# Optimization experiments

Measured on AMD Instinct MI355X. Metric: run time of the kernel, lower is better.

The kernel has to match this reference:

```python
import jax, jax.numpy as jnp
import numpy as np

B, T, D = 4, 2048, 1024
H, Dh = 16, 64
Q_LAT, KV_LAT, O_LAT = 512, 256, 512
ROPE = 32
FFN_RANK, FFN_INTER = 384, 4096
EPS = 1e-6
THETA = 10000.0


def rms_norm(x, w, eps=EPS):
    xf = x.astype(jnp.float32)
    var = jnp.mean(xf * xf, axis=-1, keepdims=True)
    return (w * (xf * jax.lax.rsqrt(var + eps))).astype(x.dtype)


def rotate_half(x):
    x1, x2 = jnp.split(x, 2, axis=-1)
    return jnp.concatenate([-x2, x1], axis=-1)


def setup_inputs() -> dict:
    key = jax.random.key(0)
    ks = jax.random.split(key, 12)
    s = lambda fan_in: 1.0 / np.sqrt(fan_in)
    inp = {
        "hidden_states": jax.random.normal(ks[0], (B, T, D), jnp.float32),
        "ln1_w": jnp.ones((D,), jnp.float32),
        "a_ln_w": jnp.ones((Q_LAT + KV_LAT,), jnp.float32),
        "qkv_a_w": jax.random.normal(ks[1], (D, Q_LAT + KV_LAT), jnp.float32) * s(D),
        "q_b_w": jax.random.normal(ks[2], (Q_LAT, H * Dh), jnp.float32) * s(Q_LAT),
        "kv_b_w": jax.random.normal(ks[3], (KV_LAT, 2 * H * Dh), jnp.float32) * s(KV_LAT),
        "o_a_w": jax.random.normal(ks[4], (H * Dh, O_LAT), jnp.float32) * s(H * Dh),
        "o_b_w": jax.random.normal(ks[5], (O_LAT, D), jnp.float32) * s(O_LAT),
        "ln2_w": jnp.ones((D,), jnp.float32),
        "ffn_in_a": jax.random.normal(ks[6], (D, FFN_RANK), jnp.float32) * s(D),
        "ffn_in_b": jax.random.normal(ks[7], (FFN_RANK, FFN_INTER), jnp.float32) * s(FFN_RANK),
        "ffn_out_a": jax.random.normal(ks[8], (FFN_INTER, FFN_RANK), jnp.float32) * s(FFN_INTER),
        "ffn_out_b": jax.random.normal(ks[9], (FFN_RANK, D), jnp.float32) * s(FFN_RANK),
    }
    # RoPE tables over first ROPE dims of each head
    inv_freq = 1.0 / (THETA ** (np.arange(0, ROPE, 2, dtype=np.float32) / ROPE))
    t = np.arange(T, dtype=np.float32)
    freqs = np.outer(t, inv_freq)                      # [T, ROPE/2]
    emb = np.concatenate([freqs, freqs], axis=-1)      # [T, ROPE]
    inp["cos"] = jnp.asarray(np.cos(emb), jnp.float32)
    inp["sin"] = jnp.asarray(np.sin(emb), jnp.float32)
    return inp


def reference(hidden_states, cos, sin, ln1_w, a_ln_w, qkv_a_w, q_b_w, kv_b_w,
              o_a_w, o_b_w, ln2_w, ffn_in_a, ffn_in_b, ffn_out_a, ffn_out_b):
    x = hidden_states
    # --- MLA attention (pre-norm) ---
    h = rms_norm(x, ln1_w)
    lat = rms_norm(h @ qkv_a_w, a_ln_w)                # [B,T,Q_LAT+KV_LAT]
    q_lat, kv_lat = jnp.split(lat, [Q_LAT], axis=-1)
    q = (q_lat @ q_b_w).reshape(B, T, H, Dh).transpose(0, 2, 1, 3)   # [B,H,T,Dh]
    kv = (kv_lat @ kv_b_w).reshape(B, T, H, 2 * Dh).transpose(0, 2, 1, 3)
    k, v = jnp.split(kv, 2, axis=-1)
    # partial RoPE on first ROPE dims
    c = cos[None, None]; s_ = sin[None, None]          # [1,1,T,ROPE]
    q_r, q_p = q[..., :ROPE], q[..., ROPE:]
    k_r, k_p = k[..., :ROPE], k[..., ROPE:]
    q = jnp.concatenate([q_r * c + rotate_half(q_r) * s_, q_p], axis=-1)
    k = jnp.concatenate([k_r * c + rotate_half(k_r) * s_, k_p], axis=-1)
    scores = jnp.einsum("bhqd,bhkd->bhqk", q, k) * (Dh ** -0.5)
    attn = jax.nn.softmax(scores, axis=-1)
    ctx = jnp.einsum("bhqk,bhkd->bhqd", attn, v)
    ctx = ctx.transpose(0, 2, 1, 3).reshape(B, T, H * Dh)
    attn_out = (ctx @ o_a_w) @ o_b_w                   # output subspace
    x = x + attn_out
    # --- decomposed FFN (pre-norm) ---
    h2 = rms_norm(x, ln2_w)
    ff = jax.nn.gelu((h2 @ ffn_in_a) @ ffn_in_b)
    ff = (ff @ ffn_out_a) @ ffn_out_b
    return x + ff
```

## Files before the change

### kernel.cpp

```cpp
#include <hip/hip_runtime.h>
#include <hip/hip_bf16.h>
#include <stdint.h>

#define NTOK 8192

typedef unsigned short u16;
typedef __attribute__((ext_vector_type(4))) float f32x4;
typedef __attribute__((ext_vector_type(8))) short s16x8;
typedef __attribute__((ext_vector_type(8))) u16   u16x8;
typedef __attribute__((ext_vector_type(4))) u16   u16x4;

__device__ __forceinline__ float fast_exp2(float x) {
    return __builtin_amdgcn_exp2f(x);
}
__device__ __forceinline__ u16 f2bf(float f) {
    uint32_t u = __float_as_uint(f);
    u = (u + 0x7FFFu + ((u >> 16) & 1u)) >> 16;
    return (u16)u;
}
__device__ __forceinline__ u16 f2bf_fast(float f) {
    return (u16)((__float_as_uint(f) + 0x8000u) >> 16);
}
__device__ __forceinline__ float bf2f(u16 h) {
    return __uint_as_float(((uint32_t)h) << 16);
}
__device__ __forceinline__ void async_cp16(const void* g, void* l) {
    __builtin_amdgcn_global_load_lds(
        (const __attribute__((address_space(1))) void*)g,
        (__attribute__((address_space(3))) void*)l, 16, 0, 0);
}
__device__ __forceinline__ void wait_vm4()   { asm volatile("s_waitcnt vmcnt(4)" ::: "memory"); }
__device__ __forceinline__ void wait_vm0()   { asm volatile("s_waitcnt vmcnt(0)" ::: "memory"); }
__device__ __forceinline__ void wait_lgkm0() { asm volatile("s_waitcnt lgkmcnt(0)" ::: "memory"); }
__device__ __forceinline__ void raw_barrier(){ asm volatile("s_barrier" ::: "memory"); }

struct TDesc { const float* s; u16* d; int K; int N; int tile0; };
struct TPack { TDesc t[8]; };

__global__ __launch_bounds__(256) void k_transpose_all(TPack p)
{
    __shared__ float tile[32][33];
    int bid = blockIdx.x;
    int i = 0;
    #pragma unroll
    for (int j = 1; j < 8; j++) if (bid >= p.t[j].tile0) i = j;
    const float* src = p.t[i].s;
    u16* dst = p.t[i].d;
    int K = p.t[i].K, N = p.t[i].N;
    int local = bid - p.t[i].tile0;
    int nx = N >> 5;
    int n0 = (local % nx) * 32, k0 = (local / nx) * 32;
    int tx = threadIdx.x, ty = threadIdx.y;
    #pragma unroll
    for (int r = 0; r < 32; r += 8)
        tile[ty + r][tx] = src[(size_t)(k0 + ty + r) * N + n0 + tx];
    __syncthreads();
    #pragma unroll
    for (int r = 0; r < 32; r += 8)
        dst[(size_t)(n0 + ty + r) * K + k0 + tx] = f2bf(tile[tx][ty + r]);
}

__global__ __launch_bounds__(256) void k_cvt(
    const float* __restrict__ in, u16* __restrict__ out)
{
    int i = (blockIdx.x * 256 + threadIdx.x) * 4;
    f32x4 v = *(const f32x4*)&in[i];
    u16x4 o;
    #pragma unroll
    for (int j = 0; j < 4; j++) o[j] = f2bf(v[j]);
    *(u16x4*)&out[i] = o;
}

template<int W>
__global__ __launch_bounds__(256) void k_rmsnorm(
    const float* __restrict__ x, const float* __restrict__ w, u16* __restrict__ out)
{
    constexpr int E = W / 256;
    int row = blockIdx.x, tid = threadIdx.x;
    const float* xr = x + (size_t)row * W;
    float v[E]; float ss = 0.f;
    #pragma unroll
    for (int i = 0; i < E; i++) { v[i] = xr[tid + i * 256]; ss += v[i] * v[i]; }
    #pragma unroll
    for (int m = 1; m < 64; m <<= 1) ss += __shfl_xor(ss, m, 64);
    __shared__ float red[4];
    if ((tid & 63) == 0) red[tid >> 6] = ss;
    __syncthreads();
    ss = red[0] + red[1] + red[2] + red[3];
    float scale = rsqrtf(ss / (float)W + 1e-6f);
    u16* orow = out + (size_t)row * W;
    #pragma unroll
    for (int i = 0; i < E; i++)
        orow[tid + i * 256] = f2bf(w[tid + i * 256] * (v[i] * scale));
}

template<int EPI>
__global__ __launch_bounds__(256) void k_gemm(
    const u16* __restrict__ A, int lda,
    const u16* __restrict__ Bt, int ldb,
    int M, int N, int K,
    float* __restrict__ outF, u16* __restrict__ outB,
    const float* __restrict__ resid)
{
    __shared__ __align__(16) u16 As[2][4096];
    __shared__ __align__(16) u16 Bs[2][4096];
    int tid = threadIdx.x;
    int w = tid >> 6, lane = tid & 63;
    int m0 = blockIdx.y * 128, n0 = blockIdx.x * 128;
    int wm = w & 1, wn = w >> 1;
    int lr = lane & 15, lq = lane >> 4;

    f32x4 acc[4][4];
    #pragma unroll
    for (int i = 0; i < 4; i++)
        #pragma unroll
        for (int j = 0; j < 4; j++) acc[i][j] = (f32x4)(0.f);

    int ar = tid >> 2;
    int ac = (tid & 3) * 8;
    const u16* Ag = A  + (size_t)(m0 + ar) * lda + ac;
    const u16* Bg = Bt + (size_t)(n0 + ar) * ldb + ac;
    int lo = w * 512;

    auto stage = [&](int kt, int s) {
        const u16* a  = Ag + kt * 32;
        const u16* bp = Bg + kt * 32;
        async_cp16(a,                     &As[s][lo]);
        async_cp16(a + (size_t)64 * lda,  &As[s][lo + 2048]);
        async_cp16(bp,                    &Bs[s][lo]);
        async_cp16(bp + (size_t)64 * ldb, &Bs[s][lo + 2048]);
    };

    int nk = K >> 5;
    stage(0, 0);
    stage(1, 1);
    for (int k = 0; k < nk; k++) {
        if (k + 1 < nk) wait_vm4(); else wait_vm0();
        raw_barrier();
        int s = k & 1;
        s16x8 af[4], bfr[4];
        #pragma unroll
        for (int ms = 0; ms < 4; ms++)
            af[ms] = *reinterpret_cast<const s16x8*>(&As[s][(wm * 64 + ms * 16 + lr) * 32 + lq * 8]);
        #pragma unroll
        for (int ns = 0; ns < 4; ns++)
            bfr[ns] = *reinterpret_cast<const s16x8*>(&Bs[s][(wn * 64 + ns * 16 + lr) * 32 + lq * 8]);
        #pragma unroll
        for (int ms = 0; ms < 4; ms++)
            #pragma unroll
            for (int ns = 0; ns < 4; ns++)
                acc[ms][ns] = __builtin_amdgcn_mfma_f32_16x16x32_bf16(af[ms], bfr[ns], acc[ms][ns], 0, 0, 0);
        wait_lgkm0();
        raw_barrier();
        if (k + 2 < nk) stage(k + 2, s);
    }

    #pragma unroll
    for (int ms = 0; ms < 4; ms++) {
        #pragma unroll
        for (int ns = 0; ns < 4; ns++) {
            int col = n0 + wn * 64 + ns * 16 + lr;
            #pragma unroll
            for (int r = 0; r < 4; r++) {
                int row = m0 + wm * 64 + ms * 16 + lq * 4 + r;
                float v = acc[ms][ns][r];
                size_t idx = (size_t)row * N + col;
                if (EPI == 0) {
                    outF[idx] = v;
                } else if (EPI == 1) {
                    outB[idx] = f2bf(v);
                } else if (EPI == 2) {
                    float t = 0.7978845608028654f * (v + 0.044715f * v * v * v);
                    outB[idx] = f2bf(0.5f * v * (1.f + tanhf(t)));
                } else {
                    outF[idx] = v + resid[idx];
                }
            }
        }
    }
}

template<int EPI>
__global__ __launch_bounds__(256) void k_gemm64(
    const u16* __restrict__ A, int lda,
    const u16* __restrict__ Bt, int ldb,
    int M, int N, int K,
    float* __restrict__ outF, u16* __restrict__ outB)
{
    __shared__ __align__(16) u16 As[2][4096];
    __shared__ __align__(16) u16 Bs[2][4096];
    int tid = threadIdx.x;
    int w = tid >> 6, lane = tid & 63;
    int m0 = blockIdx.y * 64, n0 = blockIdx.x * 64;
    int wm = w & 1, wn = w >> 1;
    int lr = lane & 15, lq = lane >> 4;

    f32x4 acc[2][2];
    #pragma unroll
    for (int i = 0; i < 2; i++)
        #pragma unroll
        for (int j = 0; j < 2; j++) acc[i][j] = (f32x4)(0.f);

    int srow = tid >> 2;
    int sq   = tid & 3;
    const u16* Ag = A  + (size_t)(m0 + srow) * lda + sq * 8;
    const u16* Bg = Bt + (size_t)(n0 + srow) * ldb + sq * 8;
    int lo = srow * 32 + sq * 8;

    auto stage = [&](int kt, int s) {
        const u16* a  = Ag + kt * 64;
        const u16* bp = Bg + kt * 64;
        async_cp16(a,       &As[s][lo]);
        async_cp16(a + 32,  &As[s][2048 + lo]);
        async_cp16(bp,      &Bs[s][lo]);
        async_cp16(bp + 32, &Bs[s][2048 + lo]);
    };

    int nk = K >> 6;
    stage(0, 0);
    stage(1, 1);
    for (int k = 0; k < nk; k++) {
        if (k + 1 < nk) wait_vm4(); else wait_vm0();
        raw_barrier();
        int s = k & 1;
        s16x8 af[2][2], bfr[2][2];
        #pragma unroll
        for (int kc = 0; kc < 2; kc++) {
            #pragma unroll
            for (int ms = 0; ms < 2; ms++)
                af[ms][kc] = *reinterpret_cast<const s16x8*>(
                    &As[s][kc * 2048 + (wm * 32 + ms * 16 + lr) * 32 + lq * 8]);
            #pragma unroll
            for (int ns = 0; ns < 2; ns++)
                bfr[ns][kc] = *reinterpret_cast<const s16x8*>(
                    &Bs[s][kc * 2048 + (wn * 32 + ns * 16 + lr) * 32 + lq * 8]);
        }
        #pragma unroll
        for (int kc = 0; kc < 2; kc++)
            #pragma unroll
            for (int ms = 0; ms < 2; ms++)
                #pragma unroll
                for (int ns = 0; ns < 2; ns++)
                    acc[ms][ns] = __builtin_amdgcn_mfma_f32_16x16x32_bf16(
                        af[ms][kc], bfr[ns][kc], acc[ms][ns], 0, 0, 0);
        wait_lgkm0();
        raw_barrier();
        if (k + 2 < nk) stage(k + 2, s);
    }

    #pragma unroll
    for (int ms = 0; ms < 2; ms++) {
        #pragma unroll
        for (int ns = 0; ns < 2; ns++) {
            int col = n0 + wn * 32 + ns * 16 + lr;
            #pragma unroll
            for (int r = 0; r < 4; r++) {
                int row = m0 + wm * 32 + ms * 16 + lq * 4 + r;
                float v = acc[ms][ns][r];
                size_t idx = (size_t)row * N + col;
                if (EPI == 0) outF[idx] = v;
                else          outB[idx] = f2bf(v);
            }
        }
    }
}

__global__ __launch_bounds__(256) void k_rope(
    const u16* __restrict__ q, const u16* __restrict__ kv,
    const float* __restrict__ cosb, const float* __restrict__ sinb,
    u16* __restrict__ q_r, u16* __restrict__ k_r)
{
    const float QS = 0.125f * 1.4426950408889634f;
    int idx = blockIdx.x * 256 + threadIdx.x;
    int g = idx & 7;
    int h = (idx >> 3) & 15;
    int t = (idx >> 7) & 2047;
    int b = idx >> 18;
    size_t qsrc = ((size_t)((b * 2048 + t) * 16 + h)) * 64 + g * 8;
    size_t ksrc = ((size_t)((b * 2048 + t) * 16 + h)) * 128 + g * 8;
    u16x8 qa = *(const u16x8*)&q[qsrc];
    u16x8 ka = *(const u16x8*)&kv[ksrc];
    u16x8 qo, ko;
    if (g < 4) {
        int pd = ((g ^ 2) - g) * 8;
        u16x8 qp = *(const u16x8*)&q[qsrc + pd];
        u16x8 kp = *(const u16x8*)&kv[ksrc + pd];
        float sgn = (g < 2) ? -1.f : 1.f;
        const float* cp = &cosb[t * 32 + g * 8];
        const float* sp = &sinb[t * 32 + g * 8];
        #pragma unroll
        for (int j = 0; j < 8; j++) {
            float c = cp[j], s = sp[j];
            qo[j] = f2bf((bf2f(qa[j]) * c + sgn * bf2f(qp[j]) * s) * QS);
            ko[j] = f2bf(bf2f(ka[j]) * c + sgn * bf2f(kp[j]) * s);
        }
    } else {
        #pragma unroll
        for (int j = 0; j < 8; j++) {
            qo[j] = f2bf(bf2f(qa[j]) * QS);
            ko[j] = ka[j];
        }
    }
    size_t dst = ((size_t)(b * 16 + h) * 2048 + t) * 64 + g * 8;
    *(u16x8*)&q_r[dst] = qo;
    *(u16x8*)&k_r[dst] = ko;
}

__global__ __launch_bounds__(256) void k_vtrans(
    const u16* __restrict__ kv, u16* __restrict__ v_t)
{
    __shared__ u16 tile[64][72];
    int bh = blockIdx.y;
    int b = bh >> 4, h = bh & 15;
    int t0 = blockIdx.x * 64;
    int tid = threadIdx.x;
    int r = tid >> 2;
    int c4 = (tid & 3) * 16;
    const u16* src = kv + ((size_t)((b * 2048 + t0 + r) * 16 + h)) * 128 + 64;
    #pragma unroll
    for (int j = 0; j < 16; j += 8)
        *(u16x8*)&tile[r][c4 + j] = *(const u16x8*)&src[c4 + j];
    __syncthreads();
    int dd = tid >> 2;
    u16* dst = v_t + ((size_t)bh * 64 + dd) * 2048 + t0;
    #pragma unroll
    for (int j0 = 0; j0 < 16; j0 += 8) {
        u16x8 vv;
        #pragma unroll
        for (int j = 0; j < 8; j++) vv[j] = tile[c4 + j0 + j][dd];
        *(u16x8*)&dst[c4 + j0] = vv;
    }
}

__global__ __launch_bounds__(256) void k_attn(
    const u16* __restrict__ q_r, const u16* __restrict__ k_r,
    const u16* __restrict__ v_t, u16* __restrict__ ctx)
{
    __shared__ __align__(16) u16 Ks[2][4096];
    __shared__ __align__(16) u16 Vs[2][4096];
    __shared__ __align__(16) u16 Ps[4][2048];
    int tid = threadIdx.x, w = tid >> 6, lane = tid & 63;
    int bh = blockIdx.y;
    int b = bh >> 4, h = bh & 15;
    int q0 = blockIdx.x * 128 + w * 32;
    const u16* Qp = q_r + (size_t)bh * 2048 * 64;
    const u16* Kp = k_r + (size_t)bh * 2048 * 64;
    const u16* Vp = v_t + (size_t)bh * 64 * 2048;
    int lr = lane & 15, lq = lane >> 4;
    int rot = (lr * 8) & 63;

    s16x8 qf[2][2];
    #pragma unroll
    for (int qc = 0; qc < 2; qc++)
        #pragma unroll
        for (int kf = 0; kf < 2; kf++)
            qf[qc][kf] = *(const s16x8*)&Qp[(size_t)(q0 + qc * 16 + lr) * 64 + kf * 32 + lq * 8];

    const u16* gstage;
    u16 *lp0, *lp1;
    size_t grow;
    if (w < 2) {
        gstage = Kp + (size_t)(lane >> 2) * 64 + w * 32 + (lane & 3) * 8;
        lp0 = &Ks[0][w * 2048]; lp1 = &Ks[1][w * 2048];
        grow = 16 * 64;
    } else {
        gstage = Vp + (size_t)(lane >> 2) * 2048 + (w - 2) * 32 + (lane & 3) * 8;
        lp0 = &Vs[0][(w - 2) * 2048]; lp1 = &Vs[1][(w - 2) * 2048];
        grow = 16 * 2048;
    }
    auto stage = [&](int kt, int s) {
        size_t goff = (w < 2) ? (size_t)kt * 64 : (size_t)kt;
        u16* lp = s ? lp1 : lp0;
        #pragma unroll
        for (int g = 0; g < 4; g++)
            async_cp16(gstage + goff + g * grow, lp + g * 512);
    };

    float l0 = 0.f, l1 = 0.f;
    f32x4 o[2][4];
    #pragma unroll
    for (int qt = 0; qt < 2; qt++)
        #pragma unroll
        for (int ds = 0; ds < 4; ds++) o[qt][ds] = (f32x4)(0.f);

    u16* Pw = Ps[w];

    stage(0, 0);
    stage(64, 1);
    for (int k = 0; k < 32; k++) {
        if (k < 31) wait_vm4(); else wait_vm0();
        raw_barrier();
        int s = k & 1;
        const u16* Ksb = Ks[s];
        const u16* Vsb = Vs[s];

        f32x4 sc[2][4];
        #pragma unroll
        for (int ns = 0; ns < 4; ns++) {
            s16x8 a0 = *(const s16x8*)&Ksb[(ns * 16 + lr) * 32 + lq * 8];
            s16x8 a1 = *(const s16x8*)&Ksb[2048 + (ns * 16 + lr) * 32 + lq * 8];
            #pragma unroll
            for (int qc = 0; qc < 2; qc++) {
                f32x4 t = (f32x4)(0.f);
                t = __builtin_amdgcn_mfma_f32_16x16x32_bf16(a0, qf[qc][0], t, 0, 0, 0);
                t = __builtin_amdgcn_mfma_f32_16x16x32_bf16(a1, qf[qc][1], t, 0, 0, 0);
                sc[qc][ns] = t;
            }
        }

        float rs0 = 0.f, rs1 = 0.f;
        #pragma unroll
        for (int ns = 0; ns < 4; ns++) {
            u16x4 pk0, pk1;
            #pragma unroll
            for (int r = 0; r < 4; r++) {
                float p0 = fast_exp2(sc[0][ns][r]);
                float p1 = fast_exp2(sc[1][ns][r]);
                rs0 += p0; rs1 += p1;
                pk0[r] = f2bf_fast(p0);
                pk1[r] = f2bf_fast(p1);
            }
            int c0 = (ns * 16 + lq * 4 + rot) & 63;
            *(u16x4*)&Pw[lr * 64 + c0] = pk0;
            *(u16x4*)&Pw[(16 + lr) * 64 + c0] = pk1;
        }
        rs0 += __shfl_xor(rs0, 16, 64);
        rs0 += __shfl_xor(rs0, 32, 64);
        rs1 += __shfl_xor(rs1, 16, 64);
        rs1 += __shfl_xor(rs1, 32, 64);
        l0 += rs0;
        l1 += rs1;

        #pragma unroll
        for (int kf = 0; kf < 2; kf++) {
            int cr = (kf * 32 + lq * 8 + rot) & 63;
            s16x8 pf0 = *(const s16x8*)&Pw[lr * 64 + cr];
            s16x8 pf1 = *(const s16x8*)&Pw[(16 + lr) * 64 + cr];
            #pragma unroll
            for (int ds = 0; ds < 4; ds++) {
                s16x8 vf = *(const s16x8*)&Vsb[kf * 2048 + (ds * 16 + lr) * 32 + lq * 8];
                o[0][ds] = __builtin_amdgcn_mfma_f32_16x16x32_bf16(pf0, vf, o[0][ds], 0, 0, 0);
                o[1][ds] = __builtin_amdgcn_mfma_f32_16x16x32_bf16(pf1, vf, o[1][ds], 0, 0, 0);
            }
        }
        wait_lgkm0();
        raw_barrier();
        if (k + 2 < 32) stage((k + 2) * 64, s);
    }

    #pragma unroll
    for (int qt = 0; qt < 2; qt++) {
        float lv = qt ? l1 : l0;
        float li[4];
        #pragma unroll
        for (int r = 0; r < 4; r++) li[r] = 1.f / __shfl(lv, lq * 4 + r, 64);
        #pragma unroll
        for (int ds = 0; ds < 4; ds++)
            #pragma unroll
            for (int r = 0; r < 4; r++) {
                int tq = q0 + qt * 16 + lq * 4 + r;
                float v = o[qt][ds][r] * li[r];
                ctx[((size_t)(b * 2048) + tq) * 1024 + h * 64 + ds * 16 + lr] = f2bf(v);
            }
    }
}

extern "C" void kernel_launch(void* const* d_in, const int* in_sizes, int n_in,
                              void* d_out, int out_size, void* d_ws, size_t ws_size,
                              hipStream_t stream) {
    (void)in_sizes; (void)n_in; (void)out_size; (void)ws_size;
    const float* x     = (const float*)d_in[0];
    const float* ln1   = (const float*)d_in[1];
    const float* alnw  = (const float*)d_in[2];
    const float* qkv_a = (const float*)d_in[3];
    const float* q_b   = (const float*)d_in[4];
    const float* kv_b  = (const float*)d_in[5];
    const float* o_a   = (const float*)d_in[6];
    const float* o_b   = (const float*)d_in[7];
    const float* ln2   = (const float*)d_in[8];
    const float* in_a  = (const float*)d_in[9];
    const float* in_b  = (const float*)d_in[10];
    const float* out_a = (const float*)d_in[11];
    const float* out_b = (const float*)d_in[12];
    const float* cosb  = (const float*)d_in[13];
    const float* sinb  = (const float*)d_in[14];
    float* out = (float*)d_out;
    char* ws = (char*)d_ws;

    u16* wqkv = (u16*)ws;
    u16* wq   = wqkv + 786432;
    u16* wkv  = wq   + 524288;
    u16* wob  = wkv  + 524288;
    u16* wia  = wob  + 524288;
    u16* wib  = wia  + 393216;
    u16* woa2 = wib  + 1572864;
    u16* wob2 = woa2 + 1572864;
    u16* woan = wob2 + 393216;
    u16* woab = woan + 524288;

    char* G = ws + 15728640;
    u16*  hbuf  = (u16*)(G + 0);
    float* lat_raw = (float*)(G + 16777216);
    u16*  lat   = (u16*)(G + 41943040);
    u16*  qbuf  = (u16*)(G + 54525952);
    u16*  kvbuf = (u16*)(G + 71303168);
    u16*  q_r   = (u16*)(G + 0);
    u16*  k_r   = (u16*)(G + 16777216);
    u16*  v_t   = (u16*)(G + 33554432);
    u16*  ctx   = (u16*)(G + 54525952);
    float* x2   = (float*)(G + 0);
    u16*  h2    = (u16*)(G + 33554432);
    u16*  t1    = (u16*)(G + 50331648);
    u16*  t2    = (u16*)(G + 56623104);
    u16*  t3    = (u16*)(G + 50331648);

    TPack tp;
    tp.t[0] = { qkv_a, wqkv, 1024, 768,  0 };
    tp.t[1] = { q_b,   wq,   512,  1024, 768 };
    tp.t[2] = { kv_b,  wkv,  256,  2048, 1280 };
    tp.t[3] = { o_b,   wob,  512,  1024, 1792 };
    tp.t[4] = { in_a,  wia,  1024, 384,  2304 };
    tp.t[5] = { in_b,  wib,  384,  4096, 2688 };
    tp.t[6] = { out_a, woa2, 4096, 384,  4224 };
    tp.t[7] = { out_b, wob2, 384,  1024, 5760 };
    k_transpose_all<<<6144, dim3(32, 8), 0, stream>>>(tp);
    k_cvt<<<512, 256, 0, stream>>>(o_a, woan);
    k_gemm64<1><<<dim3(16, 16), 256, 0, stream>>>(wob, 512, woan, 512, 1024, 1024, 512, nullptr, woab);

    k_rmsnorm<1024><<<NTOK, 256, 0, stream>>>(x, ln1, hbuf);
    k_gemm64<0><<<dim3(12, 128), 256, 0, stream>>>(hbuf, 1024, wqkv, 1024, NTOK, 768, 1024, lat_raw, nullptr);
    k_rmsnorm<768><<<NTOK, 256, 0, stream>>>(lat_raw, alnw, lat);
    k_gemm<1><<<dim3(8, 64),  256, 0, stream>>>(lat,       768, wq,  512, NTOK, 1024, 512, nullptr, qbuf,  nullptr);
    k_gemm<1><<<dim3(16, 64), 256, 0, stream>>>(lat + 512, 768, wkv, 256, NTOK, 2048, 256, nullptr, kvbuf, nullptr);
    k_rope<<<4096, 256, 0, stream>>>(qbuf, kvbuf, cosb, sinb, q_r, k_r);
    k_vtrans<<<dim3(32, 64), 256, 0, stream>>>(kvbuf, v_t);
    k_attn<<<dim3(16, 64), 256, 0, stream>>>(q_r, k_r, v_t, ctx);
    k_gemm<3><<<dim3(8, 64), 256, 0, stream>>>(ctx, 1024, woab, 1024, NTOK, 1024, 1024, x2, nullptr, x);
    k_rmsnorm<1024><<<NTOK, 256, 0, stream>>>(x2, ln2, h2);
    k_gemm64<1><<<dim3(6, 128), 256, 0, stream>>>(h2, 1024, wia, 1024, NTOK, 384, 1024, nullptr, t1);
    k_gemm<2><<<dim3(32, 64), 256, 0, stream>>>(t1, 384, wib, 384, NTOK, 4096, 384, nullptr, t2, nullptr);
    k_gemm64<1><<<dim3(6, 128), 256, 0, stream>>>(t2, 4096, woa2, 4096, NTOK, 384, 4096, nullptr, t3);
    k_gemm<3><<<dim3(8, 64), 256, 0, stream>>>(t3, 384, wob2, 384, NTOK, 1024, 384, out, nullptr, x2);
}
```

Before: 546.4 us.

## Keep attention P in registers and XOR-swizzle K/V shared tiles

Drops the per-wave shared-memory round trip for the softmax probabilities. The score accumulator layout is fed directly as the MFMA A operand, and the V fragments are gathered from two 4-element reads to match that key permutation. It also XOR-swizzles the 16-byte chunks when staging K and V into LDS, to cut bank conflicts on the fragment reads. This removes LDS writes and reads plus a dependency stall per tile, at the cost of split V loads and more complex indexing.

```diff
diff --git a/kernel.cpp b/kernel.cpp
--- a/kernel.cpp
+++ b/kernel.cpp
@@ -7,6 +7,7 @@
 typedef unsigned short u16;
 typedef __attribute__((ext_vector_type(4))) float f32x4;
 typedef __attribute__((ext_vector_type(8))) short s16x8;
+typedef __attribute__((ext_vector_type(4))) short s16x4;
 typedef __attribute__((ext_vector_type(8))) u16   u16x8;
 typedef __attribute__((ext_vector_type(4))) u16   u16x4;
 
@@ -338,7 +339,6 @@
 {
     __shared__ __align__(16) u16 Ks[2][4096];
     __shared__ __align__(16) u16 Vs[2][4096];
-    __shared__ __align__(16) u16 Ps[4][2048];
     int tid = threadIdx.x, w = tid >> 6, lane = tid & 63;
     int bh = blockIdx.y;
     int b = bh >> 4, h = bh & 15;
@@ -347,7 +347,7 @@
     const u16* Kp = k_r + (size_t)bh * 2048 * 64;
     const u16* Vp = v_t + (size_t)bh * 64 * 2048;
     int lr = lane & 15, lq = lane >> 4;
-    int rot = (lr * 8) & 63;
+    int swz = (lr >> 1) & 3;
 
     s16x8 qf[2][2];
     #pragma unroll
@@ -356,15 +356,16 @@
         for (int kf = 0; kf < 2; kf++)
             qf[qc][kf] = *(const s16x8*)&Qp[(size_t)(q0 + qc * 16 + lr) * 64 + kf * 32 + lq * 8];
 
+    int schunk = ((lane & 3) ^ ((lane >> 3) & 3)) * 8;
     const u16* gstage;
     u16 *lp0, *lp1;
     size_t grow;
     if (w < 2) {
-        gstage = Kp + (size_t)(lane >> 2) * 64 + w * 32 + (lane & 3) * 8;
+        gstage = Kp + (size_t)(lane >> 2) * 64 + w * 32 + schunk;
         lp0 = &Ks[0][w * 2048]; lp1 = &Ks[1][w * 2048];
         grow = 16 * 64;
     } else {
-        gstage = Vp + (size_t)(lane >> 2) * 2048 + (w - 2) * 32 + (lane & 3) * 8;
+        gstage = Vp + (size_t)(lane >> 2) * 2048 + (w - 2) * 32 + schunk;
         lp0 = &Vs[0][(w - 2) * 2048]; lp1 = &Vs[1][(w - 2) * 2048];
         grow = 16 * 2048;
     }
@@ -382,8 +383,6 @@
     for (int qt = 0; qt < 2; qt++)
         #pragma unroll
         for (int ds = 0; ds < 4; ds++) o[qt][ds] = (f32x4)(0.f);
-
-    u16* Pw = Ps[w];
 
     stage(0, 0);
     stage(64, 1);
@@ -397,8 +396,9 @@
         f32x4 sc[2][4];
         #pragma unroll
         for (int ns = 0; ns < 4; ns++) {
-            s16x8 a0 = *(const s16x8*)&Ksb[(ns * 16 + lr) * 32 + lq * 8];
-            s16x8 a1 = *(const s16x8*)&Ksb[2048 + (ns * 16 + lr) * 32 + lq * 8];
+            int ko = (ns * 16 + lr) * 32 + ((lq ^ swz) * 8);
+            s16x8 a0 = *(const s16x8*)&Ksb[ko];
+            s16x8 a1 = *(const s16x8*)&Ksb[2048 + ko];
             #pragma unroll
             for (int qc = 0; qc < 2; qc++) {
                 f32x4 t = (f32x4)(0.f);
@@ -410,19 +410,29 @@
 
         float rs0 = 0.f, rs1 = 0.f;
         #pragma unroll
-        for (int ns = 0; ns < 4; ns++) {
-            u16x4 pk0, pk1;
-            #pragma unroll
-            for (int r = 0; r < 4; r++) {
-                float p0 = fast_exp2(sc[0][ns][r]);
-                float p1 = fast_exp2(sc[1][ns][r]);
-                rs0 += p0; rs1 += p1;
-                pk0[r] = f2bf_fast(p0);
-                pk1[r] = f2bf_fast(p1);
+        for (int kf = 0; kf < 2; kf++) {
+            s16x8 pk0, pk1;
+            #pragma unroll
+            for (int hh = 0; hh < 2; hh++) {
+                int ns = kf * 2 + hh;
+                #pragma unroll
+                for (int r = 0; r < 4; r++) {
+                    float p0 = fast_exp2(sc[0][ns][r]);
+                    float p1 = fast_exp2(sc[1][ns][r]);
+                    rs0 += p0; rs1 += p1;
+                    pk0[hh * 4 + r] = (short)f2bf_fast(p0);
+                    pk1[hh * 4 + r] = (short)f2bf_fast(p1);
+                }
             }
-            int c0 = (ns * 16 + lq * 4 + rot) & 63;
-            *(u16x4*)&Pw[lr * 64 + c0] = pk0;
-            *(u16x4*)&Pw[(16 + lr) * 64 + c0] = pk1;
+            #pragma unroll
+            for (int ds = 0; ds < 4; ds++) {
+                int vbase = kf * 2048 + (ds * 16 + lr) * 32 + (lq & 1) * 4;
+                s16x4 vlo = *(const s16x4*)&Vsb[vbase + (((lq >> 1)    ) ^ swz) * 8];
+                s16x4 vhi = *(const s16x4*)&Vsb[vbase + (((lq >> 1) | 2) ^ swz) * 8];
+                s16x8 vf = __builtin_shufflevector(vlo, vhi, 0, 1, 2, 3, 4, 5, 6, 7);
+                o[0][ds] = __builtin_amdgcn_mfma_f32_16x16x32_bf16(pk0, vf, o[0][ds], 0, 0, 0);
+                o[1][ds] = __builtin_amdgcn_mfma_f32_16x16x32_bf16(pk1, vf, o[1][ds], 0, 0, 0);
+            }
         }
         rs0 += __shfl_xor(rs0, 16, 64);
         rs0 += __shfl_xor(rs0, 32, 64);
@@ -431,18 +441,6 @@
         l0 += rs0;
         l1 += rs1;
 
-        #pragma unroll
-        for (int kf = 0; kf < 2; kf++) {
-            int cr = (kf * 32 + lq * 8 + rot) & 63;
-            s16x8 pf0 = *(const s16x8*)&Pw[lr * 64 + cr];
-            s16x8 pf1 = *(const s16x8*)&Pw[(16 + lr) * 64 + cr];
-            #pragma unroll
-            for (int ds = 0; ds < 4; ds++) {
-                s16x8 vf = *(const s16x8*)&Vsb[kf * 2048 + (ds * 16 + lr) * 32 + lq * 8];
-                o[0][ds] = __builtin_amdgcn_mfma_f32_16x16x32_bf16(pf0, vf, o[0][ds], 0, 0, 0);
-                o[1][ds] = __builtin_amdgcn_mfma_f32_16x16x32_bf16(pf1, vf, o[1][ds], 0, 0, 0);
-            }
-        }
         wait_lgkm0();
         raw_barrier();
         if (k + 2 < 32) stage((k + 2) * 64, s);
```

Result: no change. 539.3 us (-1.3%).
